# Optimization experiments

Hardware: AMD Instinct MI355X
Metric: run time of the kernel (lower is better)

## Reference

```python
import jax, jax.numpy as jnp
import numpy as np

B, T, F_IN, H = 128, 512, 128, 128
EPS = 1e-5


def setup_inputs() -> dict:
    key = jax.random.key(0)
    ks = jax.random.split(key, 24)
    s = 0.05
    r = lambda k, shp: jax.random.normal(k, shp, jnp.float32) * s
    return {
        "x": jax.random.normal(ks[0], (B, T, F_IN), jnp.float32),
        "group_labels": jax.random.randint(ks[1], (B,), 0, 4),
        "conv1_w": r(ks[2], (64, F_IN, 3)), "conv1_b": jnp.zeros((64,), jnp.float32),
        "bn1_g": jnp.ones((64,), jnp.float32), "bn1_b": jnp.zeros((64,), jnp.float32),
        "conv2_w": r(ks[3], (128, 64, 3)), "conv2_b": jnp.zeros((128,), jnp.float32),
        "bn2_g": jnp.ones((128,), jnp.float32), "bn2_b": jnp.zeros((128,), jnp.float32),
        "wih0": r(ks[4], (2, 4 * H, 128)), "whh0": r(ks[5], (2, 4 * H, H)), "b0": r(ks[6], (2, 4 * H)),
        "wih1": r(ks[7], (2, 4 * H, 2 * H)), "whh1": r(ks[8], (2, 4 * H, H)), "b1": r(ks[9], (2, 4 * H)),
        "att_w": r(ks[10], (2 * H,)), "att_b": r(ks[11], (1,)),
        "dec_w1": r(ks[12], (4, 64, 2 * H)), "dec_b1": r(ks[13], (4, 64)),
        "dec_w2": r(ks[14], (4, 32, 64)), "dec_b2": r(ks[15], (4, 32)),
        "dec_w3": r(ks[16], (4, 1, 32)), "dec_b3": r(ks[17], (4, 1)),
    }


def _bn(x, g, b):
    # training-mode batch stats over (N, L) per channel; x: (B, C, L)
    m = x.mean(axis=(0, 2), keepdims=True)
    v = x.var(axis=(0, 2), keepdims=True)
    return (x - m) / jnp.sqrt(v + EPS) * g[None, :, None] + b[None, :, None]


def _conv1d(x, w, b):
    # x: (B, C, L), w: (O, I, 3), padding=1
    y = jax.lax.conv_general_dilated(x, w, (1,), ((1, 1),), dimension_numbers=("NCH", "OIH", "NCH"))
    return y + b[None, :, None]


def _lstm_dir(x, wih, whh, b, reverse):
    Bv, Hv = x.shape[0], whh.shape[1]
    xg = jnp.einsum("btd,gd->btg", x, wih) + b  # precomputed input gates (B, T, 4H)

    def step(carry, xt):
        h, c = carry
        gates = xt + h @ whh.T
        i, f, g, o = jnp.split(gates, 4, axis=-1)  # torch gate order i,f,g,o
        c = jax.nn.sigmoid(f) * c + jax.nn.sigmoid(i) * jnp.tanh(g)
        h = jax.nn.sigmoid(o) * jnp.tanh(c)
        return (h, c), h

    init = (jnp.zeros((Bv, Hv), x.dtype), jnp.zeros((Bv, Hv), x.dtype))
    _, hs = jax.lax.scan(step, init, jnp.swapaxes(xg, 0, 1), reverse=reverse)
    return jnp.swapaxes(hs, 0, 1)  # (B, T, H), time-aligned for both directions


def _bilstm(x, wih, whh, b):
    hf = _lstm_dir(x, wih[0], whh[0], b[0], False)
    hb = _lstm_dir(x, wih[1], whh[1], b[1], True)
    return jnp.concatenate([hf, hb], axis=-1)


def reference(x, group_labels, conv1_w, conv1_b, bn1_g, bn1_b, conv2_w, conv2_b,
              bn2_g, bn2_b, wih0, whh0, b0, wih1, whh1, b1, att_w, att_b,
              dec_w1, dec_b1, dec_w2, dec_b2, dec_w3, dec_b3):
    # ---- shared encoder ----
    h = jnp.swapaxes(x, 1, 2)                          # (B, F, T)
    h = jax.nn.relu(_bn(_conv1d(h, conv1_w, conv1_b), bn1_g, bn1_b))
    h = jax.nn.relu(_bn(_conv1d(h, conv2_w, conv2_b), bn2_g, bn2_b))
    h = jnp.swapaxes(h, 1, 2)                          # (B, T, 128)
    h = _bilstm(h, wih0, whh0, b0)                     # (B, T, 2H)
    h = _bilstm(h, wih1, whh1, b1)                     # (B, T, 2H)
    scores = h @ att_w + att_b                         # (B, T)
    attn = jax.nn.softmax(scores, axis=1)
    attended = jnp.einsum("bt,btd->bd", attn, h)       # (B, 2H)
    # ---- group-routed decoders (batch=1 per sample in original => BN skipped) ----
    h1 = jax.nn.relu(jnp.einsum("bd,ehd->beh", attended, dec_w1) + dec_b1[None])   # (B,4,64)
    h2 = jax.nn.relu(jnp.einsum("beh,egh->beg", h1, dec_w2) + dec_b2[None])         # (B,4,32)
    outs = jnp.einsum("beg,eog->beo", h2, dec_w3) + dec_b3[None]                    # (B,4,1)
    preds = jnp.take_along_axis(outs[:, :, 0], group_labels[:, None], axis=1)       # (B,1)
    return preds, attn
```

## Files before the change

### kernel.cpp

```cpp
#include <hip/hip_runtime.h>
#include <hip/hip_bf16.h>

#define EPS_ 1e-5f

typedef __attribute__((ext_vector_type(4))) float f32x4;
typedef __attribute__((ext_vector_type(8))) short s16x8;
typedef __attribute__((ext_vector_type(4))) short s16x4;
typedef unsigned short u16;

static __device__ __forceinline__ u16 f2bf(float f) {
  __hip_bfloat16 h = __float2bfloat16(f);
  return *reinterpret_cast<u16*>(&h);
}
static __device__ __forceinline__ float bf2f(u16 u) {
  union { float f; unsigned int i; } v; v.i = ((unsigned int)u) << 16; return v.f;
}
static __device__ __forceinline__ float sigf(float x) {
  return __builtin_amdgcn_rcpf(1.f + __expf(-x));
}
static __device__ __forceinline__ float tanhf_(float x) {
  return 2.f * __builtin_amdgcn_rcpf(1.f + __expf(-2.f * x)) - 1.f;
}
static __device__ __forceinline__ f32x4 mfma16(s16x8 a, s16x8 b, f32x4 c) {
  return __builtin_amdgcn_mfma_f32_16x16x32_bf16(a, b, c, 0, 0, 0);
}

__global__ void convw_kernel(const float* __restrict__ src, u16* __restrict__ dst,
                             int KIN, int ksbits, int total) {
  int i = blockIdx.x * 256 + threadIdx.x;
  if (i >= total) return;
  int e = i & 7;
  int lane = (i >> 3) & 63;
  int w = (i >> 9) & 7;
  int g = (i >> 12) & 3;
  int t2 = i >> 14;
  int ks = t2 & ((1 << ksbits) - 1);
  int d = t2 >> ksbits;
  int r = g * 128 + w * 16 + (lane & 15);
  int k = ks * 32 + (lane >> 4) * 8 + e;
  dst[i] = f2bf(src[((size_t)d * 512 + r) * KIN + k]);
}

__global__ void transw_kernel(const float* __restrict__ src, float* __restrict__ dst,
                              int IC, int OC, int total) {
  int n = blockIdx.x * 256 + threadIdx.x;
  if (n >= total) return;
  int oc = n % OC;
  int r = n / OC;
  int i = r % IC;
  int tap = r / IC;
  dst[n] = src[(oc * IC + i) * 3 + tap];
}

template<int IC, int OC, bool HASBN>
__global__ __launch_bounds__(256) void conv_kernel(
    const float* __restrict__ xin, const float* __restrict__ wt,
    const float* __restrict__ bsrc, const float* __restrict__ stats_in,
    const float* __restrict__ g_in, const float* __restrict__ beta_in,
    float* __restrict__ yout, float* __restrict__ stats_out) {
  constexpr int OCPT = OC / 4;
  __shared__ float xlds[66][IC + 1];
  __shared__ float insc[IC], insh[IC];

  const int tid = threadIdx.x;
  const int b = blockIdx.x >> 3;
  const int t0 = (blockIdx.x & 7) * 64;

  if constexpr (HASBN) {
    for (int c = tid; c < IC; c += 256) {
      float s0 = stats_in[2 * c], s1 = stats_in[2 * c + 1];
      float m = s0 * (1.f / 65536.f);
      float v = s1 * (1.f / 65536.f) - m * m;
      float inv = rsqrtf(v + EPS_);
      float a = g_in[c] * inv;
      insc[c] = a; insh[c] = beta_in[c] - m * a;
    }
    __syncthreads();
  }

  for (int n = tid; n < 66 * (IC / 4); n += 256) {
    int row = n / (IC / 4);
    int c4 = (n % (IC / 4)) * 4;
    int t = t0 + row - 1;
    float v0 = 0.f, v1 = 0.f, v2 = 0.f, v3 = 0.f;
    if (t >= 0 && t < 512) {
      f32x4 v = *(const f32x4*)&xin[((size_t)b * 512 + t) * IC + c4];
      v0 = v[0]; v1 = v[1]; v2 = v[2]; v3 = v[3];
      if constexpr (HASBN) {
        v0 = fmaxf(v0 * insc[c4 + 0] + insh[c4 + 0], 0.f);
        v1 = fmaxf(v1 * insc[c4 + 1] + insh[c4 + 1], 0.f);
        v2 = fmaxf(v2 * insc[c4 + 2] + insh[c4 + 2], 0.f);
        v3 = fmaxf(v3 * insc[c4 + 3] + insh[c4 + 3], 0.f);
      }
    }
    xlds[row][c4 + 0] = v0; xlds[row][c4 + 1] = v1;
    xlds[row][c4 + 2] = v2; xlds[row][c4 + 3] = v3;
  }
  __syncthreads();

  const int tt = tid & 63;
  const int ocb = (tid >> 6) * OCPT;
  float acc[OCPT];
#pragma unroll
  for (int j = 0; j < OCPT; ++j) acc[j] = 0.f;

#pragma unroll
  for (int tap = 0; tap < 3; ++tap) {
    const float* xr = &xlds[tt + tap][0];
    const float* wr0 = &wt[(size_t)tap * IC * OC + ocb];
#pragma unroll 4
    for (int i = 0; i < IC; ++i) {
      float xv = xr[i];
      const float* wr = wr0 + i * OC;
#pragma unroll
      for (int j4 = 0; j4 < OCPT; j4 += 4) {
        f32x4 wv = *(const f32x4*)&wr[j4];
        acc[j4 + 0] = fmaf(xv, wv[0], acc[j4 + 0]);
        acc[j4 + 1] = fmaf(xv, wv[1], acc[j4 + 1]);
        acc[j4 + 2] = fmaf(xv, wv[2], acc[j4 + 2]);
        acc[j4 + 3] = fmaf(xv, wv[3], acc[j4 + 3]);
      }
    }
  }

  const int t = t0 + tt;
#pragma unroll
  for (int j = 0; j < OCPT; ++j) acc[j] += bsrc[ocb + j];
  float* yr = &yout[((size_t)b * 512 + t) * OC + ocb];
#pragma unroll
  for (int j4 = 0; j4 < OCPT; j4 += 4) {
    f32x4 o; o[0] = acc[j4]; o[1] = acc[j4 + 1]; o[2] = acc[j4 + 2]; o[3] = acc[j4 + 3];
    *(f32x4*)&yr[j4] = o;
  }

#pragma unroll
  for (int j = 0; j < OCPT; ++j) {
    float s = acc[j];
    float qv = s * s;
#pragma unroll
    for (int m = 32; m > 0; m >>= 1) {
      s += __shfl_xor(s, m, 64);
      qv += __shfl_xor(qv, m, 64);
    }
    if ((tid & 63) == 0) {
      atomicAdd(&stats_out[2 * (ocb + j)], s);
      atomicAdd(&stats_out[2 * (ocb + j) + 1], qv);
    }
  }
}

template<int KIN, bool BN>
__global__ __launch_bounds__(512, 1) void xg_kernel(
    const void* __restrict__ xin_, const float* __restrict__ stats,
    const float* __restrict__ bng, const float* __restrict__ bnb,
    const u16* __restrict__ wihP, const float* __restrict__ bias,
    u16* __restrict__ xgo) {
  constexpr int NKS = KIN / 32;
  constexpr int XSTR = KIN + 8;
  __shared__ u16 xl[2][16][XSTR];
  __shared__ float sc[128], sh[128];

  const int tid = threadIdx.x;
  const int wv = tid >> 6, lane = tid & 63, q = lane >> 4, col = lane & 15;
  const int bid = blockIdx.x;
  const int dir = bid >> 7, bg = (bid >> 4) & 7, t0 = (bid & 15) * 32;
  const int b0 = bg * 16;
  const int ss = tid >> 5, cc = tid & 31;
  const float* xf = (const float*)xin_;
  const u16* xh = (const u16*)xin_;

  if constexpr (BN) {
    for (int c = tid; c < 128; c += 512) {
      float s0 = stats[2 * c], s1 = stats[2 * c + 1];
      float m = s0 * (1.f / 65536.f);
      float v = s1 * (1.f / 65536.f) - m * m;
      float inv = rsqrtf(v + EPS_);
      float a = bng[c] * inv;
      sc[c] = a; sh[c] = bnb[c] - m * a;
    }
    __syncthreads();
  }

  const s16x8* wihv = (const s16x8*)wihP;
  s16x8 aw[NKS][4];
#pragma unroll
  for (int ks = 0; ks < NKS; ++ks)
#pragma unroll
    for (int g = 0; g < 4; ++g)
      aw[ks][g] = wihv[(((dir * NKS + ks) * 4 + g) * 8 + wv) * 64 + lane];

  f32x4 bias4[4];
#pragma unroll
  for (int g = 0; g < 4; ++g)
    bias4[g] = *(const f32x4*)&bias[dir * 512 + g * 128 + wv * 16 + q * 4];

  if constexpr (KIN == 128) {
    f32x4 v = *(const f32x4*)&xf[((size_t)(b0 + ss) * 512 + t0) * 128 + cc * 4];
    s16x4 u;
#pragma unroll
    for (int j = 0; j < 4; ++j) {
      float xx = v[j];
      if constexpr (BN) xx = fmaxf(xx * sc[cc * 4 + j] + sh[cc * 4 + j], 0.f);
      u[j] = (short)f2bf(xx);
    }
    *(s16x4*)&xl[0][ss][cc * 4] = u;
  } else {
    *(s16x8*)&xl[0][ss][cc * 8] =
        *(const s16x8*)&xh[((size_t)(b0 + ss) * 512 + t0) * 256 + cc * 8];
  }
  __syncthreads();

  int cur = 0;
  for (int i = 0; i < 32; ++i) {
    const int t = t0 + i;
    const int tn = t0 + ((i < 31) ? i + 1 : 31);
    f32x4 xnf; s16x8 xnh;
    if constexpr (KIN == 128)
      xnf = *(const f32x4*)&xf[((size_t)(b0 + ss) * 512 + tn) * 128 + cc * 4];
    else
      xnh = *(const s16x8*)&xh[((size_t)(b0 + ss) * 512 + tn) * 256 + cc * 8];

    s16x8 bx[NKS];
#pragma unroll
    for (int ks = 0; ks < NKS; ++ks)
      bx[ks] = *(const s16x8*)&xl[cur][col][ks * 32 + q * 8];

    f32x4 a0 = bias4[0], a1 = bias4[1], a2 = bias4[2], a3 = bias4[3];
#pragma unroll
    for (int ks = 0; ks < NKS; ++ks) {
      a0 = mfma16(aw[ks][0], bx[ks], a0);
      a1 = mfma16(aw[ks][1], bx[ks], a1);
      a2 = mfma16(aw[ks][2], bx[ks], a2);
      a3 = mfma16(aw[ks][3], bx[ks], a3);
    }

    u16* op = xgo + (((size_t)((dir * 8 + bg) * 512 + t)) * 32 + wv * 4) * 256
            + (size_t)lane * 4;
#define STORE_G(G, A)                                              \
    { s16x4 o;                                                     \
      o[0] = (short)f2bf(A[0]); o[1] = (short)f2bf(A[1]);          \
      o[2] = (short)f2bf(A[2]); o[3] = (short)f2bf(A[3]);          \
      *(s16x4*)(op + G * 256) = o; }
    STORE_G(0, a0) STORE_G(1, a1) STORE_G(2, a2) STORE_G(3, a3)
#undef STORE_G

    if constexpr (KIN == 128) {
      s16x4 u;
#pragma unroll
      for (int j = 0; j < 4; ++j) {
        float xx = xnf[j];
        if constexpr (BN) xx = fmaxf(xx * sc[cc * 4 + j] + sh[cc * 4 + j], 0.f);
        u[j] = (short)f2bf(xx);
      }
      *(s16x4*)&xl[cur ^ 1][ss][cc * 4] = u;
    } else {
      *(s16x8*)&xl[cur ^ 1][ss][cc * 8] = xnh;
    }
    __syncthreads();
    cur ^= 1;
  }
}

__global__ __launch_bounds__(512, 1) void lstm_kernel(
    const u16* __restrict__ whhP, const u16* __restrict__ xg,
    u16* __restrict__ hout) {
  __shared__ u16 hl[2][16][136];
  const int tid = threadIdx.x;
  const int wv = tid >> 6, lane = tid & 63, q = lane >> 4, col = lane & 15;
  const int dir = blockIdx.x >> 3, bg = blockIdx.x & 7, b0 = bg * 16;

  for (int n = tid; n < 16 * 136; n += 512) (&hl[0][0][0])[n] = 0;

  const s16x8* whhv = (const s16x8*)whhP;
  s16x8 awhh[4][4];
#pragma unroll
  for (int ks = 0; ks < 4; ++ks)
#pragma unroll
    for (int g = 0; g < 4; ++g)
      awhh[ks][g] = whhv[(((dir * 4 + ks) * 4 + g) * 8 + wv) * 64 + lane];

  const u16* xgp = xg + ((size_t)(dir * 8 + bg)) * 512 * 8192
                 + (size_t)(wv * 4) * 256 + (size_t)lane * 4;

  const int tstep = dir ? -1 : 1;
  int t = dir ? 511 : 0;

  s16x4 xn0 = *(const s16x4*)(xgp + (size_t)t * 8192);
  s16x4 xn1 = *(const s16x4*)(xgp + (size_t)t * 8192 + 256);
  s16x4 xn2 = *(const s16x4*)(xgp + (size_t)t * 8192 + 512);
  s16x4 xn3 = *(const s16x4*)(xgp + (size_t)t * 8192 + 768);

  __syncthreads();

  float c0 = 0.f, c1 = 0.f, c2 = 0.f, c3 = 0.f;
  int cur = 0;

  for (int it = 0; it < 512; ++it) {
    s16x4 xc0 = xn0, xc1 = xn1, xc2 = xn2, xc3 = xn3;
    const int tn = (it < 511) ? t + tstep : t;
    xn0 = *(const s16x4*)(xgp + (size_t)tn * 8192);
    xn1 = *(const s16x4*)(xgp + (size_t)tn * 8192 + 256);
    xn2 = *(const s16x4*)(xgp + (size_t)tn * 8192 + 512);
    xn3 = *(const s16x4*)(xgp + (size_t)tn * 8192 + 768);

    s16x8 bh[4];
#pragma unroll
    for (int ks = 0; ks < 4; ++ks)
      bh[ks] = *(const s16x8*)&hl[cur][col][ks * 32 + q * 8];

    f32x4 a0, a1, a2, a3;
#pragma unroll
    for (int e = 0; e < 4; ++e) {
      a0[e] = bf2f((u16)xc0[e]); a1[e] = bf2f((u16)xc1[e]);
      a2[e] = bf2f((u16)xc2[e]); a3[e] = bf2f((u16)xc3[e]);
    }
#pragma unroll
    for (int ks = 0; ks < 4; ++ks) {
      a0 = mfma16(awhh[ks][0], bh[ks], a0);
      a1 = mfma16(awhh[ks][1], bh[ks], a1);
      a2 = mfma16(awhh[ks][2], bh[ks], a2);
      a3 = mfma16(awhh[ks][3], bh[ks], a3);
    }

    f32x4 hn;
#define GATE_STEP(E, CP)                                            \
    {                                                               \
      float sI = sigf(a0[E]); float sF = sigf(a1[E]);               \
      float tG = tanhf_(a2[E]); float sO = sigf(a3[E]);             \
      float cn = sF * CP + sI * tG;                                 \
      CP = cn;                                                      \
      hn[E] = sO * tanhf_(cn);                                      \
    }
    GATE_STEP(0, c0) GATE_STEP(1, c1) GATE_STEP(2, c2) GATE_STEP(3, c3)
#undef GATE_STEP

    s16x4 hb;
#pragma unroll
    for (int e = 0; e < 4; ++e) hb[e] = (short)f2bf(hn[e]);
    *(s16x4*)&hout[((size_t)(b0 + col) * 512 + t) * 256 + dir * 128 + wv * 16 + q * 4] = hb;
    *(s16x4*)&hl[cur ^ 1][col][wv * 16 + q * 4] = hb;

    asm volatile("s_waitcnt lgkmcnt(0)" ::: "memory");
    __builtin_amdgcn_sched_barrier(0);
    __builtin_amdgcn_s_barrier();
    __builtin_amdgcn_sched_barrier(0);

    cur ^= 1;
    t += tstep;
  }
}

__global__ __launch_bounds__(256) void attn_kernel(
    const u16* __restrict__ h1, const float* __restrict__ attw,
    const float* __restrict__ attb, float* __restrict__ out_attn,
    float* __restrict__ attended) {
  const int b = blockIdx.x;
  const int tid = threadIdx.x;
  const int w = tid >> 6, l = tid & 63;
  __shared__ float sl[512];
  __shared__ float red[256];
  __shared__ float red2[4][256];

  f32x4 wv4 = *(const f32x4*)&attw[l * 4];
  const float ab = attb[0];
  for (int i = 0; i < 128; ++i) {
    int t = w * 128 + i;
    s16x4 v = *(const s16x4*)&h1[((size_t)b * 512 + t) * 256 + l * 4];
    float s = bf2f((u16)v[0]) * wv4[0] + bf2f((u16)v[1]) * wv4[1]
            + bf2f((u16)v[2]) * wv4[2] + bf2f((u16)v[3]) * wv4[3];
#pragma unroll
    for (int m = 32; m > 0; m >>= 1) s += __shfl_xor(s, m, 64);
    if (l == 0) sl[t] = s + ab;
  }
  __syncthreads();

  red[tid] = fmaxf(sl[tid], sl[tid + 256]);
  __syncthreads();
  for (int st = 128; st > 0; st >>= 1) {
    if (tid < st) red[tid] = fmaxf(red[tid], red[tid + st]);
    __syncthreads();
  }
  const float mx = red[0];
  __syncthreads();

  float e0 = __expf(sl[tid] - mx);
  float e1 = __expf(sl[tid + 256] - mx);
  sl[tid] = e0; sl[tid + 256] = e1;
  red[tid] = e0 + e1;
  __syncthreads();
  for (int st = 128; st > 0; st >>= 1) {
    if (tid < st) red[tid] += red[tid + st];
    __syncthreads();
  }
  const float inv = 1.f / red[0];

  out_attn[(size_t)b * 512 + tid] = sl[tid] * inv;
  out_attn[(size_t)b * 512 + tid + 256] = sl[tid + 256] * inv;
  __syncthreads();

  float a0 = 0.f, a1 = 0.f, a2 = 0.f, a3 = 0.f;
  for (int i = 0; i < 128; ++i) {
    int t = w * 128 + i;
    float p = sl[t] * inv;
    s16x4 v = *(const s16x4*)&h1[((size_t)b * 512 + t) * 256 + l * 4];
    a0 += p * bf2f((u16)v[0]); a1 += p * bf2f((u16)v[1]);
    a2 += p * bf2f((u16)v[2]); a3 += p * bf2f((u16)v[3]);
  }
  red2[w][l * 4 + 0] = a0; red2[w][l * 4 + 1] = a1;
  red2[w][l * 4 + 2] = a2; red2[w][l * 4 + 3] = a3;
  __syncthreads();
  attended[b * 256 + tid] =
      red2[0][tid] + red2[1][tid] + red2[2][tid] + red2[3][tid];
}

__global__ __launch_bounds__(64) void dec_kernel(
    const float* __restrict__ attended, const int* __restrict__ labels,
    const float* __restrict__ w1, const float* __restrict__ b1,
    const float* __restrict__ w2, const float* __restrict__ b2,
    const float* __restrict__ w3, const float* __restrict__ b3,
    float* __restrict__ preds) {
  const int b = blockIdx.x;
  const int tid = threadIdx.x;
  const int g = labels[b];
  __shared__ float al[256];
  __shared__ float hl1[64];
  __shared__ float hl2[32];

  for (int i = tid; i < 256; i += 64) al[i] = attended[b * 256 + i];
  __syncthreads();

  {
    const float* wr = &w1[(size_t)(g * 64 + tid) * 256];
    float a = b1[g * 64 + tid];
    for (int d = 0; d < 256; d += 4) {
      f32x4 wv = *(const f32x4*)&wr[d];
      a += al[d] * wv[0] + al[d + 1] * wv[1] + al[d + 2] * wv[2] + al[d + 3] * wv[3];
    }
    hl1[tid] = fmaxf(a, 0.f);
  }
  __syncthreads();
  if (tid < 32) {
    const float* wr = &w2[(size_t)(g * 32 + tid) * 64];
    float a = b2[g * 32 + tid];
    for (int d = 0; d < 64; d += 4) {
      f32x4 wv = *(const f32x4*)&wr[d];
      a += hl1[d] * wv[0] + hl1[d + 1] * wv[1] + hl1[d + 2] * wv[2] + hl1[d + 3] * wv[3];
    }
    hl2[tid] = fmaxf(a, 0.f);
  }
  __syncthreads();
  if (tid < 32) {
    float a = hl2[tid] * w3[g * 32 + tid];
#pragma unroll
    for (int m = 16; m > 0; m >>= 1) a += __shfl_xor(a, m, 32);
    if (tid == 0) preds[b] = a + b3[g];
  }
}

extern "C" void kernel_launch(void* const* d_in, const int* in_sizes, int n_in,
                              void* d_out, int out_size, void* d_ws, size_t ws_size,
                              hipStream_t stream) {
  const float* x      = (const float*)d_in[0];
  const int*   labels = (const int*)d_in[1];
  const float* conv1w = (const float*)d_in[2];
  const float* conv1b = (const float*)d_in[3];
  const float* bn1g   = (const float*)d_in[4];
  const float* bn1b   = (const float*)d_in[5];
  const float* conv2w = (const float*)d_in[6];
  const float* conv2b = (const float*)d_in[7];
  const float* bn2g   = (const float*)d_in[8];
  const float* bn2b   = (const float*)d_in[9];
  const float* wih0   = (const float*)d_in[10];
  const float* whh0   = (const float*)d_in[11];
  const float* b0     = (const float*)d_in[12];
  const float* wih1   = (const float*)d_in[13];
  const float* whh1   = (const float*)d_in[14];
  const float* b1     = (const float*)d_in[15];
  const float* attw   = (const float*)d_in[16];
  const float* attb   = (const float*)d_in[17];
  const float* dw1    = (const float*)d_in[18];
  const float* db1    = (const float*)d_in[19];
  const float* dw2    = (const float*)d_in[20];
  const float* db2    = (const float*)d_in[21];
  const float* dw3    = (const float*)d_in[22];
  const float* db3    = (const float*)d_in[23];

  char* ws = (char*)d_ws;
  u16*   whh0P = (u16*)  (ws + 0x000000);
  u16*   whh1P = (u16*)  (ws + 0x040000);
  u16*   wih0P = (u16*)  (ws + 0x080000);
  u16*   wih1P = (u16*)  (ws + 0x0C0000);
  float* wt1   = (float*)(ws + 0x140000);
  float* wt2   = (float*)(ws + 0x158000);
  float* st1   = (float*)(ws + 0x170000);
  float* st2   = (float*)(ws + 0x170200);
  float* attd  = (float*)(ws + 0x170600);
  u16*   h0    = (u16*)  (ws + 0x200000);
  float* y2    = (float*)(ws + 0x2200000);
  u16*   h1    = (u16*)  (ws + 0x2200000);
  u16*   xgb   = (u16*)  (ws + 0x4200000);
  float* y1    = (float*)(ws + 0x4200000);

  float* preds    = (float*)d_out;
  float* attn_out = (float*)d_out + 128;

  hipMemsetAsync(ws + 0x170000, 0, 0x600, stream);

  convw_kernel<<<512, 256, 0, stream>>>(wih0, wih0P, 128, 2, 131072);
  convw_kernel<<<512, 256, 0, stream>>>(whh0, whh0P, 128, 2, 131072);
  convw_kernel<<<1024, 256, 0, stream>>>(wih1, wih1P, 256, 3, 262144);
  convw_kernel<<<512, 256, 0, stream>>>(whh1, whh1P, 128, 2, 131072);
  transw_kernel<<<96, 256, 0, stream>>>(conv1w, wt1, 128, 64, 24576);
  transw_kernel<<<96, 256, 0, stream>>>(conv2w, wt2, 64, 128, 24576);

  conv_kernel<128, 64, false><<<1024, 256, 0, stream>>>(
      x, wt1, conv1b, nullptr, nullptr, nullptr, y1, st1);
  conv_kernel<64, 128, true><<<1024, 256, 0, stream>>>(
      y1, wt2, conv2b, st1, bn1g, bn1b, y2, st2);

  xg_kernel<128, true><<<256, 512, 0, stream>>>(
      y2, st2, bn2g, bn2b, wih0P, b0, xgb);
  lstm_kernel<<<16, 512, 0, stream>>>(whh0P, xgb, h0);
  xg_kernel<256, false><<<256, 512, 0, stream>>>(
      h0, nullptr, nullptr, nullptr, wih1P, b1, xgb);
  lstm_kernel<<<16, 512, 0, stream>>>(whh1P, xgb, h1);

  attn_kernel<<<128, 256, 0, stream>>>(h1, attw, attb, attn_out, attd);
  dec_kernel<<<128, 64, 0, stream>>>(attd, labels, dw1, db1, dw2, db2, dw3, db3, preds);
}
```

Baseline: 2.121 ms.

## Run conv layers on bf16 MFMA with packed weights and swizzled LDS

Replaces the scalar fp32 FMA conv1d kernels with kernels that treat each conv as a GEMM over (tap, input channel) and use 16x16x32 bf16 MFMA. Weights are pre-packed into bf16 MFMA fragments held in registers. Inputs are staged in LDS as bf16 with an XOR swizzle to avoid bank conflicts. BN statistics are now reduced per 16-lane group before the atomics. This cuts conv compute cost but drops input and weight precision to bf16 and adds rounding error to the BN statistics. The LSTM recurrence probably dominates total time anyway.

```diff
diff --git a/kernel.cpp b/kernel.cpp
--- a/kernel.cpp
+++ b/kernel.cpp
@@ -41,33 +41,42 @@
   dst[i] = f2bf(src[((size_t)d * 512 + r) * KIN + k]);
 }
 
-__global__ void transw_kernel(const float* __restrict__ src, float* __restrict__ dst,
-                              int IC, int OC, int total) {
-  int n = blockIdx.x * 256 + threadIdx.x;
-  if (n >= total) return;
-  int oc = n % OC;
-  int r = n / OC;
-  int i = r % IC;
-  int tap = r / IC;
-  dst[n] = src[(oc * IC + i) * 3 + tap];
-}
-
-template<int IC, int OC, bool HASBN>
-__global__ __launch_bounds__(256) void conv_kernel(
-    const float* __restrict__ xin, const float* __restrict__ wt,
+__global__ void convwf_kernel(const float* __restrict__ src, u16* __restrict__ dst,
+                              int IC, int NW, int total) {
+  int i = blockIdx.x * 256 + threadIdx.x;
+  if (i >= total) return;
+  int e = i & 7;
+  int lane = (i >> 3) & 63;
+  int blk = i >> 9;
+  int wb = blk % NW;
+  int ks = blk / NW;
+  int oc = wb * 16 + (lane & 15);
+  int k = ks * 32 + (lane >> 4) * 8 + e;
+  int tap = k / IC;
+  int ic = k - tap * IC;
+  dst[i] = f2bf(src[(oc * IC + ic) * 3 + tap]);
+}
+
+template<int IC, int NW, bool BN>
+__global__ __launch_bounds__(512, 1) void convm_kernel(
+    const float* __restrict__ xin, const u16* __restrict__ wP,
     const float* __restrict__ bsrc, const float* __restrict__ stats_in,
     const float* __restrict__ g_in, const float* __restrict__ beta_in,
     float* __restrict__ yout, float* __restrict__ stats_out) {
-  constexpr int OCPT = OC / 4;
-  __shared__ float xlds[66][IC + 1];
+  constexpr int OC = NW * 16;
+  constexpr int NKS = (3 * IC) / 32;
+  constexpr int ICQ = IC / 32;
+  __shared__ u16 xs[66 * IC];
   __shared__ float insc[IC], insh[IC];
 
   const int tid = threadIdx.x;
+  const int wv = tid >> 6, lane = tid & 63, q = lane >> 4, col = lane & 15;
   const int b = blockIdx.x >> 3;
   const int t0 = (blockIdx.x & 7) * 64;
-
-  if constexpr (HASBN) {
-    for (int c = tid; c < IC; c += 256) {
+  char* xsb = (char*)xs;
+
+  if constexpr (BN) {
+    for (int c = tid; c < IC; c += 512) {
       float s0 = stats_in[2 * c], s1 = stats_in[2 * c + 1];
       float m = s0 * (1.f / 65536.f);
       float v = s1 * (1.f / 65536.f) - m * m;
@@ -78,74 +87,81 @@
     __syncthreads();
   }
 
-  for (int n = tid; n < 66 * (IC / 4); n += 256) {
-    int row = n / (IC / 4);
+  for (int n = tid; n < 66 * (IC / 4); n += 512) {
+    int r = n / (IC / 4);
     int c4 = (n % (IC / 4)) * 4;
-    int t = t0 + row - 1;
+    int t = t0 + r - 1;
     float v0 = 0.f, v1 = 0.f, v2 = 0.f, v3 = 0.f;
     if (t >= 0 && t < 512) {
       f32x4 v = *(const f32x4*)&xin[((size_t)b * 512 + t) * IC + c4];
       v0 = v[0]; v1 = v[1]; v2 = v[2]; v3 = v[3];
-      if constexpr (HASBN) {
+      if constexpr (BN) {
         v0 = fmaxf(v0 * insc[c4 + 0] + insh[c4 + 0], 0.f);
         v1 = fmaxf(v1 * insc[c4 + 1] + insh[c4 + 1], 0.f);
         v2 = fmaxf(v2 * insc[c4 + 2] + insh[c4 + 2], 0.f);
         v3 = fmaxf(v3 * insc[c4 + 3] + insh[c4 + 3], 0.f);
       }
     }
-    xlds[row][c4 + 0] = v0; xlds[row][c4 + 1] = v1;
-    xlds[row][c4 + 2] = v2; xlds[row][c4 + 3] = v3;
-  }
-  __syncthreads();
-
-  const int tt = tid & 63;
-  const int ocb = (tid >> 6) * OCPT;
-  float acc[OCPT];
-#pragma unroll
-  for (int j = 0; j < OCPT; ++j) acc[j] = 0.f;
-
-#pragma unroll
-  for (int tap = 0; tap < 3; ++tap) {
-    const float* xr = &xlds[tt + tap][0];
-    const float* wr0 = &wt[(size_t)tap * IC * OC + ocb];
-#pragma unroll 4
-    for (int i = 0; i < IC; ++i) {
-      float xv = xr[i];
-      const float* wr = wr0 + i * OC;
-#pragma unroll
-      for (int j4 = 0; j4 < OCPT; j4 += 4) {
-        f32x4 wv = *(const f32x4*)&wr[j4];
-        acc[j4 + 0] = fmaf(xv, wv[0], acc[j4 + 0]);
-        acc[j4 + 1] = fmaf(xv, wv[1], acc[j4 + 1]);
-        acc[j4 + 2] = fmaf(xv, wv[2], acc[j4 + 2]);
-        acc[j4 + 3] = fmaf(xv, wv[3], acc[j4 + 3]);
-      }
-    }
-  }
-
-  const int t = t0 + tt;
-#pragma unroll
-  for (int j = 0; j < OCPT; ++j) acc[j] += bsrc[ocb + j];
-  float* yr = &yout[((size_t)b * 512 + t) * OC + ocb];
-#pragma unroll
-  for (int j4 = 0; j4 < OCPT; j4 += 4) {
-    f32x4 o; o[0] = acc[j4]; o[1] = acc[j4 + 1]; o[2] = acc[j4 + 2]; o[3] = acc[j4 + 3];
-    *(f32x4*)&yr[j4] = o;
-  }
-
-#pragma unroll
-  for (int j = 0; j < OCPT; ++j) {
-    float s = acc[j];
-    float qv = s * s;
-#pragma unroll
-    for (int m = 32; m > 0; m >>= 1) {
-      s += __shfl_xor(s, m, 64);
-      qv += __shfl_xor(qv, m, 64);
-    }
-    if ((tid & 63) == 0) {
-      atomicAdd(&stats_out[2 * (ocb + j)], s);
-      atomicAdd(&stats_out[2 * (ocb + j) + 1], qv);
-    }
+    s16x4 u;
+    u[0] = (short)f2bf(v0); u[1] = (short)f2bf(v1);
+    u[2] = (short)f2bf(v2); u[3] = (short)f2bf(v3);
+    int byte = ((r * IC + c4) * 2) ^ ((r & 7) << 4);
+    *(s16x4*)(xsb + byte) = u;
+  }
+  __syncthreads();
+
+  const int wb = (NW == 8) ? wv : (wv & 3);
+  const s16x8* wPv = (const s16x8*)wP;
+  s16x8 aA[NKS];
+#pragma unroll
+  for (int ks = 0; ks < NKS; ++ks)
+    aA[ks] = wPv[(ks * NW + wb) * 64 + lane];
+
+  f32x4 bias4 = *(const f32x4*)&bsrc[wb * 16 + q * 4];
+
+  constexpr int NSUB = (NW == 8) ? 4 : 2;
+  const int st0 = (NW == 8) ? 0 : ((wv >> 2) * 2);
+
+  float ssum0 = 0.f, ssum1 = 0.f, ssum2 = 0.f, ssum3 = 0.f;
+  float ssq0 = 0.f, ssq1 = 0.f, ssq2 = 0.f, ssq3 = 0.f;
+
+#pragma unroll
+  for (int s = 0; s < NSUB; ++s) {
+    const int tbase = (st0 + s) * 16;
+    const int t_loc = tbase + col;
+    f32x4 acc = bias4;
+#pragma unroll
+    for (int ks = 0; ks < NKS; ++ks) {
+      const int tap = ks / ICQ;
+      const int icb = (ks % ICQ) * 32 + q * 8;
+      const int R = t_loc + tap;
+      int byte = ((R * IC + icb) * 2) ^ ((R & 7) << 4);
+      s16x8 bB = *(const s16x8*)(xsb + byte);
+      acc = mfma16(aA[ks], bB, acc);
+    }
+    *(f32x4*)&yout[((size_t)b * 512 + t0 + t_loc) * OC + wb * 16 + q * 4] = acc;
+    ssum0 += acc[0]; ssq0 += acc[0] * acc[0];
+    ssum1 += acc[1]; ssq1 += acc[1] * acc[1];
+    ssum2 += acc[2]; ssq2 += acc[2] * acc[2];
+    ssum3 += acc[3]; ssq3 += acc[3] * acc[3];
+  }
+
+#define RED16(S)                                   \
+  S += __shfl_xor(S, 1, 64); S += __shfl_xor(S, 2, 64); \
+  S += __shfl_xor(S, 4, 64); S += __shfl_xor(S, 8, 64);
+  RED16(ssum0) RED16(ssum1) RED16(ssum2) RED16(ssum3)
+  RED16(ssq0)  RED16(ssq1)  RED16(ssq2)  RED16(ssq3)
+#undef RED16
+  if (col == 0) {
+    const int ocb = wb * 16 + q * 4;
+    atomicAdd(&stats_out[2 * (ocb + 0)], ssum0);
+    atomicAdd(&stats_out[2 * (ocb + 0) + 1], ssq0);
+    atomicAdd(&stats_out[2 * (ocb + 1)], ssum1);
+    atomicAdd(&stats_out[2 * (ocb + 1) + 1], ssq1);
+    atomicAdd(&stats_out[2 * (ocb + 2)], ssum2);
+    atomicAdd(&stats_out[2 * (ocb + 2) + 1], ssq2);
+    atomicAdd(&stats_out[2 * (ocb + 3)], ssum3);
+    atomicAdd(&stats_out[2 * (ocb + 3) + 1], ssq3);
   }
 }
 
@@ -490,8 +506,8 @@
   u16*   whh1P = (u16*)  (ws + 0x040000);
   u16*   wih0P = (u16*)  (ws + 0x080000);
   u16*   wih1P = (u16*)  (ws + 0x0C0000);
-  float* wt1   = (float*)(ws + 0x140000);
-  float* wt2   = (float*)(ws + 0x158000);
+  u16*   cw1P  = (u16*)  (ws + 0x140000);
+  u16*   cw2P  = (u16*)  (ws + 0x150000);
   float* st1   = (float*)(ws + 0x170000);
   float* st2   = (float*)(ws + 0x170200);
   float* attd  = (float*)(ws + 0x170600);
@@ -510,13 +526,13 @@
   convw_kernel<<<512, 256, 0, stream>>>(whh0, whh0P, 128, 2, 131072);
   convw_kernel<<<1024, 256, 0, stream>>>(wih1, wih1P, 256, 3, 262144);
   convw_kernel<<<512, 256, 0, stream>>>(whh1, whh1P, 128, 2, 131072);
-  transw_kernel<<<96, 256, 0, stream>>>(conv1w, wt1, 128, 64, 24576);
-  transw_kernel<<<96, 256, 0, stream>>>(conv2w, wt2, 64, 128, 24576);
-
-  conv_kernel<128, 64, false><<<1024, 256, 0, stream>>>(
-      x, wt1, conv1b, nullptr, nullptr, nullptr, y1, st1);
-  conv_kernel<64, 128, true><<<1024, 256, 0, stream>>>(
-      y1, wt2, conv2b, st1, bn1g, bn1b, y2, st2);
+  convwf_kernel<<<96, 256, 0, stream>>>(conv1w, cw1P, 128, 4, 24576);
+  convwf_kernel<<<96, 256, 0, stream>>>(conv2w, cw2P, 64, 8, 24576);
+
+  convm_kernel<128, 4, false><<<1024, 512, 0, stream>>>(
+      x, cw1P, conv1b, nullptr, nullptr, nullptr, y1, st1);
+  convm_kernel<64, 8, true><<<1024, 512, 0, stream>>>(
+      y1, cw2P, conv2b, st1, bn1g, bn1b, y2, st2);
 
   xg_kernel<128, true><<<256, 512, 0, stream>>>(
       y2, st2, bn2g, bn2b, wih0P, b0, xgb);
```

After: 1.752 ms. 1.21x faster.
